# Kernel tuning notes

Measured on AMD Instinct MI355X. Metric: run time of the kernel, lower is better.

Reference implementation:

```python
import jax, jax.numpy as jnp
import numpy as np
import math

CH = 64  # channel

def setup_inputs() -> dict:
    key = jax.random.key(0)
    ks = jax.random.split(key, 7)
    B, K, M = 4, 32, 8192
    grouped_xyz = jax.random.normal(ks[0], (B, 3, K, M), dtype=jnp.float32)
    s = 1.0 / math.sqrt(3.0)
    Wq = jax.random.uniform(ks[1], (CH, 3), jnp.float32, -s, s)
    bq = jax.random.uniform(ks[2], (CH,), jnp.float32, -s, s)
    Wk = jax.random.uniform(ks[3], (CH, 3), jnp.float32, -s, s)
    bk = jax.random.uniform(ks[4], (CH,), jnp.float32, -s, s)
    Wv = jax.random.uniform(ks[5], (CH, 3), jnp.float32, -s, s)
    bv = jax.random.uniform(ks[6], (CH,), jnp.float32, -s, s)
    return {"grouped_xyz": grouped_xyz, "Wq": Wq, "bq": bq, "Wk": Wk, "bk": bk, "Wv": Wv, "bv": bv}

def reference(grouped_xyz, Wq, bq, Wk, bk, Wv, bv):
    # 1x1 conv = channel-wise linear: (B,3,K,M) -> (B,M,K,CH) after permute (0,3,2,1)
    def proj(W, b):
        return jnp.einsum('oc,bckm->bmko', W, grouped_xyz) + b
    q = proj(Wq, bq)  # B,M,K,C
    k = proj(Wk, bk)
    v = proj(Wv, bv)
    score = jnp.einsum('bmkc,bmjc->bmkj', q, k) / math.sqrt(CH)
    attn = jax.nn.softmax(score, axis=-1)
    pe = jax.nn.relu(jnp.einsum('bmkj,bmjc->bmkc', attn, v))  # B,M,K,C
    return pe
```

## Files before the change

### kernel.cpp

```cpp
#include <hip/hip_runtime.h>
#include <cstdint>

#define M_TOT 8192
#define K_PTS 32
#define NCH 64
#define MT 16

__global__ void setup_kernel(const float* __restrict__ Wq, const float* __restrict__ bq,
                             const float* __restrict__ Wk, const float* __restrict__ bk,
                             float* __restrict__ ws) {
  if (threadIdx.x == 0 && blockIdx.x == 0) {
    const float scale = 1.4426950408889634f / 8.0f;
    float A[9] = {0,0,0,0,0,0,0,0,0};
    float u[3] = {0,0,0};
    for (int o = 0; o < NCH; ++o) {
      float wq0 = Wq[o*3+0], wq1 = Wq[o*3+1], wq2 = Wq[o*3+2];
      float wk0 = Wk[o*3+0], wk1 = Wk[o*3+1], wk2 = Wk[o*3+2];
      float bqo = bq[o];
      A[0] += wq0*wk0; A[1] += wq0*wk1; A[2] += wq0*wk2;
      A[3] += wq1*wk0; A[4] += wq1*wk1; A[5] += wq1*wk2;
      A[6] += wq2*wk0; A[7] += wq2*wk1; A[8] += wq2*wk2;
      u[0] += bqo*wk0; u[1] += bqo*wk1; u[2] += bqo*wk2;
    }
    for (int i = 0; i < 9; ++i) ws[i] = A[i] * scale;
    for (int i = 0; i < 3; ++i) ws[9+i] = u[i] * scale;
  }
}

__global__ __launch_bounds__(512) void attn_main(const float* __restrict__ xyz,
                                                 const float* __restrict__ Wv,
                                                 const float* __restrict__ bv,
                                                 const float* __restrict__ ws,
                                                 float* __restrict__ out) {
  __shared__ __align__(16) float x_lds[MT*97 + 4];
  __shared__ __align__(16) float gh_lds[MT*128];
  __shared__ __align__(16) float y_lds[MT*128];

  const int t = threadIdx.x;
  const int b = blockIdx.x >> 9;
  const int m0 = (blockIdx.x & 511) * MT;

  const float* xb = xyz + ((size_t)b * 3 * K_PTS) * M_TOT + m0;

  #pragma unroll
  for (int p = 0; p < 3; ++p) {
    int i = t + p * 512;
    int mo = i & (MT - 1);
    int r  = i >> 4;
    float val = xb[(size_t)r * M_TOT + mo];
    int k = r & 31, c = r >> 5;
    x_lds[mo*97 + k*3 + c] = val;
  }

  float A00 = ws[0], A01 = ws[1], A02 = ws[2];
  float A10 = ws[3], A11 = ws[4], A12 = ws[5];
  float A20 = ws[6], A21 = ws[7], A22 = ws[8];
  float u0  = ws[9], u1  = ws[10], u2 = ws[11];

  __syncthreads();

  {
    int m = t >> 5, j = t & 31;
    float x0 = x_lds[m*97 + j*3 + 0];
    float x1 = x_lds[m*97 + j*3 + 1];
    float x2 = x_lds[m*97 + j*3 + 2];
    float g0 = fmaf(A02, x2, fmaf(A01, x1, A00 * x0));
    float g1 = fmaf(A12, x2, fmaf(A11, x1, A10 * x0));
    float g2 = fmaf(A22, x2, fmaf(A21, x1, A20 * x0));
    float h  = fmaf(u2,  x2, fmaf(u1,  x1, u0  * x0));
    *(float4*)&gh_lds[m*128 + j*4] = make_float4(g0, g1, g2, h);
  }
  __syncthreads();

  {
    int m = t >> 5, k = t & 31;
    float xk0 = x_lds[m*97 + k*3 + 0];
    float xk1 = x_lds[m*97 + k*3 + 1];
    float xk2 = x_lds[m*97 + k*3 + 2];
    float s[32];
    #pragma unroll
    for (int j = 0; j < 32; ++j) {
      float4 gh = *(const float4*)&gh_lds[m*128 + j*4];
      s[j] = fmaf(xk0, gh.x, fmaf(xk1, gh.y, fmaf(xk2, gh.z, gh.w)));
    }
    float mx = s[0];
    #pragma unroll
    for (int j = 1; j < 32; ++j) mx = fmaxf(mx, s[j]);
    float sum = 0.f, y0 = 0.f, y1 = 0.f, y2 = 0.f;
    #pragma unroll
    for (int j = 0; j < 32; ++j) {
      float p = exp2f(s[j] - mx);
      sum += p;
      y0 = fmaf(p, x_lds[m*97 + j*3 + 0], y0);
      y1 = fmaf(p, x_lds[m*97 + j*3 + 1], y1);
      y2 = fmaf(p, x_lds[m*97 + j*3 + 2], y2);
    }
    float inv = 1.0f / sum;
    *(float4*)&y_lds[m*128 + k*4] = make_float4(y0*inv, y1*inv, y2*inv, 0.f);
  }
  __syncthreads();

  {
    int k  = t >> 4;
    int c4 = (t & 15) * 4;
    float w00 = Wv[(c4+0)*3+0], w01 = Wv[(c4+0)*3+1], w02 = Wv[(c4+0)*3+2], b0 = bv[c4+0];
    float w10 = Wv[(c4+1)*3+0], w11 = Wv[(c4+1)*3+1], w12 = Wv[(c4+1)*3+2], b1 = bv[c4+1];
    float w20 = Wv[(c4+2)*3+0], w21 = Wv[(c4+2)*3+1], w22 = Wv[(c4+2)*3+2], b2 = bv[c4+2];
    float w30 = Wv[(c4+3)*3+0], w31 = Wv[(c4+3)*3+1], w32 = Wv[(c4+3)*3+2], b3 = bv[c4+3];
    float* op = out + (((size_t)b * M_TOT + m0) * K_PTS + k) * NCH + c4;
    #pragma unroll
    for (int m = 0; m < MT; ++m) {
      float4 y = *(const float4*)&y_lds[m*128 + k*4];
      float4 r;
      r.x = fmaxf(0.f, fmaf(w00, y.x, fmaf(w01, y.y, fmaf(w02, y.z, b0))));
      r.y = fmaxf(0.f, fmaf(w10, y.x, fmaf(w11, y.y, fmaf(w12, y.z, b1))));
      r.z = fmaxf(0.f, fmaf(w20, y.x, fmaf(w21, y.y, fmaf(w22, y.z, b2))));
      r.w = fmaxf(0.f, fmaf(w30, y.x, fmaf(w31, y.y, fmaf(w32, y.z, b3))));
      *(float4*)(op + (size_t)m * (K_PTS * NCH)) = r;
    }
  }
}

extern "C" void kernel_launch(void* const* d_in, const int* in_sizes, int n_in,
                              void* d_out, int out_size, void* d_ws, size_t ws_size,
                              hipStream_t stream) {
  const float* xyz = (const float*)d_in[0];
  const float* Wq  = (const float*)d_in[1];
  const float* bq  = (const float*)d_in[2];
  const float* Wk  = (const float*)d_in[3];
  const float* bk  = (const float*)d_in[4];
  const float* Wv  = (const float*)d_in[5];
  const float* bv  = (const float*)d_in[6];
  float* out = (float*)d_out;
  float* ws  = (float*)d_ws;

  setup_kernel<<<1, 64, 0, stream>>>(Wq, bq, Wk, bk, ws);
  attn_main<<<2048, 512, 0, stream>>>(xyz, Wv, bv, ws, out);
}
```

Measured before the change: 60.69 us.

## Fuse weight-precompute into main kernel and shrink tile to 8 points

Removes the single-thread setup kernel by having every block compute the folded Wq^T Wk matrix and bias vector via wavefront xor-shuffle reductions, eliminating one launch and its serialization. The tile is halved to 8 points with 256-thread blocks (4096 blocks), scores are recomputed in a second pass instead of held in a 32-entry register array, and output stores become nontemporal. This trades redundant per-block reduction work and recomputed dot products for lower register pressure, more blocks, and no inter-kernel dependency.

```diff
diff --git a/kernel.cpp b/kernel.cpp
--- a/kernel.cpp
+++ b/kernel.cpp
@@ -4,59 +4,67 @@
 #define M_TOT 8192
 #define K_PTS 32
 #define NCH 64
-#define MT 16
+#define MT 8
 
-__global__ void setup_kernel(const float* __restrict__ Wq, const float* __restrict__ bq,
-                             const float* __restrict__ Wk, const float* __restrict__ bk,
-                             float* __restrict__ ws) {
-  if (threadIdx.x == 0 && blockIdx.x == 0) {
-    const float scale = 1.4426950408889634f / 8.0f;
-    float A[9] = {0,0,0,0,0,0,0,0,0};
-    float u[3] = {0,0,0};
-    for (int o = 0; o < NCH; ++o) {
-      float wq0 = Wq[o*3+0], wq1 = Wq[o*3+1], wq2 = Wq[o*3+2];
-      float wk0 = Wk[o*3+0], wk1 = Wk[o*3+1], wk2 = Wk[o*3+2];
-      float bqo = bq[o];
-      A[0] += wq0*wk0; A[1] += wq0*wk1; A[2] += wq0*wk2;
-      A[3] += wq1*wk0; A[4] += wq1*wk1; A[5] += wq1*wk2;
-      A[6] += wq2*wk0; A[7] += wq2*wk1; A[8] += wq2*wk2;
-      u[0] += bqo*wk0; u[1] += bqo*wk1; u[2] += bqo*wk2;
-    }
-    for (int i = 0; i < 9; ++i) ws[i] = A[i] * scale;
-    for (int i = 0; i < 3; ++i) ws[9+i] = u[i] * scale;
-  }
-}
+typedef float f4 __attribute__((ext_vector_type(4)));
 
-__global__ __launch_bounds__(512) void attn_main(const float* __restrict__ xyz,
-                                                 const float* __restrict__ Wv,
-                                                 const float* __restrict__ bv,
-                                                 const float* __restrict__ ws,
-                                                 float* __restrict__ out) {
+__global__ __launch_bounds__(256) void attn_fused(const float* __restrict__ xyz,
+                                                  const float* __restrict__ Wq,
+                                                  const float* __restrict__ bq,
+                                                  const float* __restrict__ Wk,
+                                                  const float* __restrict__ Wv,
+                                                  const float* __restrict__ bv,
+                                                  float* __restrict__ out) {
   __shared__ __align__(16) float x_lds[MT*97 + 4];
   __shared__ __align__(16) float gh_lds[MT*128];
   __shared__ __align__(16) float y_lds[MT*128];
 
   const int t = threadIdx.x;
-  const int b = blockIdx.x >> 9;
-  const int m0 = (blockIdx.x & 511) * MT;
+  const int b = blockIdx.x >> 10;
+  const int m0 = (blockIdx.x & 1023) * MT;
 
   const float* xb = xyz + ((size_t)b * 3 * K_PTS) * M_TOT + m0;
 
+  float xv[3];
+  int rr[3], mm[3];
   #pragma unroll
   for (int p = 0; p < 3; ++p) {
-    int i = t + p * 512;
-    int mo = i & (MT - 1);
-    int r  = i >> 4;
-    float val = xb[(size_t)r * M_TOT + mo];
-    int k = r & 31, c = r >> 5;
-    x_lds[mo*97 + k*3 + c] = val;
+    int i = t + p * 256;
+    mm[p] = i & (MT - 1);
+    rr[p] = i >> 3;
+    xv[p] = xb[(size_t)rr[p] * M_TOT + mm[p]];
   }
 
-  float A00 = ws[0], A01 = ws[1], A02 = ws[2];
-  float A10 = ws[3], A11 = ws[4], A12 = ws[5];
-  float A20 = ws[6], A21 = ws[7], A22 = ws[8];
-  float u0  = ws[9], u1  = ws[10], u2 = ws[11];
+  const int c4 = (t & 15) * 4;
+  float w00 = Wv[(c4+0)*3+0], w01 = Wv[(c4+0)*3+1], w02 = Wv[(c4+0)*3+2], bv0 = bv[c4+0];
+  float w10 = Wv[(c4+1)*3+0], w11 = Wv[(c4+1)*3+1], w12 = Wv[(c4+1)*3+2], bv1 = bv[c4+1];
+  float w20 = Wv[(c4+2)*3+0], w21 = Wv[(c4+2)*3+1], w22 = Wv[(c4+2)*3+2], bv2 = bv[c4+2];
+  float w30 = Wv[(c4+3)*3+0], w31 = Wv[(c4+3)*3+1], w32 = Wv[(c4+3)*3+2], bv3 = bv[c4+3];
 
+  const int o = t & 63;
+  float wq0 = Wq[o*3+0], wq1 = Wq[o*3+1], wq2 = Wq[o*3+2];
+  float wk0 = Wk[o*3+0], wk1 = Wk[o*3+1], wk2 = Wk[o*3+2];
+  float bqo = bq[o];
+  float A00 = wq0*wk0, A01 = wq0*wk1, A02 = wq0*wk2;
+  float A10 = wq1*wk0, A11 = wq1*wk1, A12 = wq1*wk2;
+  float A20 = wq2*wk0, A21 = wq2*wk1, A22 = wq2*wk2;
+  float u0 = bqo*wk0, u1 = bqo*wk1, u2 = bqo*wk2;
+  #pragma unroll
+  for (int st = 1; st < 64; st <<= 1) {
+    A00 += __shfl_xor(A00, st); A01 += __shfl_xor(A01, st); A02 += __shfl_xor(A02, st);
+    A10 += __shfl_xor(A10, st); A11 += __shfl_xor(A11, st); A12 += __shfl_xor(A12, st);
+    A20 += __shfl_xor(A20, st); A21 += __shfl_xor(A21, st); A22 += __shfl_xor(A22, st);
+    u0  += __shfl_xor(u0,  st); u1  += __shfl_xor(u1,  st); u2  += __shfl_xor(u2,  st);
+  }
+  const float sc = 1.4426950408889634f / 8.0f;
+  A00 *= sc; A01 *= sc; A02 *= sc; A10 *= sc; A11 *= sc; A12 *= sc;
+  A20 *= sc; A21 *= sc; A22 *= sc; u0 *= sc; u1 *= sc; u2 *= sc;
+
+  #pragma unroll
+  for (int p = 0; p < 3; ++p) {
+    int k = rr[p] & 31, c = rr[p] >> 5;
+    x_lds[mm[p]*97 + k*3 + c] = xv[p];
+  }
   __syncthreads();
 
   {
@@ -68,7 +76,7 @@
     float g1 = fmaf(A12, x2, fmaf(A11, x1, A10 * x0));
     float g2 = fmaf(A22, x2, fmaf(A21, x1, A20 * x0));
     float h  = fmaf(u2,  x2, fmaf(u1,  x1, u0  * x0));
-    *(float4*)&gh_lds[m*128 + j*4] = make_float4(g0, g1, g2, h);
+    *(f4*)&gh_lds[m*128 + j*4] = (f4){g0, g1, g2, h};
   }
   __syncthreads();
 
@@ -77,46 +85,44 @@
     float xk0 = x_lds[m*97 + k*3 + 0];
     float xk1 = x_lds[m*97 + k*3 + 1];
     float xk2 = x_lds[m*97 + k*3 + 2];
-    float s[32];
+    float mx = -3.4e38f;
     #pragma unroll
     for (int j = 0; j < 32; ++j) {
-      float4 gh = *(const float4*)&gh_lds[m*128 + j*4];
-      s[j] = fmaf(xk0, gh.x, fmaf(xk1, gh.y, fmaf(xk2, gh.z, gh.w)));
+      f4 gh = *(const f4*)&gh_lds[m*128 + j*4];
+      float s = fmaf(xk0, gh.x, fmaf(xk1, gh.y, fmaf(xk2, gh.z, gh.w)));
+      mx = fmaxf(mx, s);
     }
-    float mx = s[0];
-    #pragma unroll
-    for (int j = 1; j < 32; ++j) mx = fmaxf(mx, s[j]);
     float sum = 0.f, y0 = 0.f, y1 = 0.f, y2 = 0.f;
     #pragma unroll
     for (int j = 0; j < 32; ++j) {
-      float p = exp2f(s[j] - mx);
+      f4 gh = *(const f4*)&gh_lds[m*128 + j*4];
+      float s = fmaf(xk0, gh.x, fmaf(xk1, gh.y, fmaf(xk2, gh.z, gh.w)));
+      float p = exp2f(s - mx);
       sum += p;
       y0 = fmaf(p, x_lds[m*97 + j*3 + 0], y0);
       y1 = fmaf(p, x_lds[m*97 + j*3 + 1], y1);
       y2 = fmaf(p, x_lds[m*97 + j*3 + 2], y2);
     }
     float inv = 1.0f / sum;
-    *(float4*)&y_lds[m*128 + k*4] = make_float4(y0*inv, y1*inv, y2*inv, 0.f);
+    *(f4*)&y_lds[m*128 + k*4] = (f4){y0*inv, y1*inv, y2*inv, 0.f};
   }
   __syncthreads();
 
   {
-    int k  = t >> 4;
-    int c4 = (t & 15) * 4;
-    float w00 = Wv[(c4+0)*3+0], w01 = Wv[(c4+0)*3+1], w02 = Wv[(c4+0)*3+2], b0 = bv[c4+0];
-    float w10 = Wv[(c4+1)*3+0], w11 = Wv[(c4+1)*3+1], w12 = Wv[(c4+1)*3+2], b1 = bv[c4+1];
-    float w20 = Wv[(c4+2)*3+0], w21 = Wv[(c4+2)*3+1], w22 = Wv[(c4+2)*3+2], b2 = bv[c4+2];
-    float w30 = Wv[(c4+3)*3+0], w31 = Wv[(c4+3)*3+1], w32 = Wv[(c4+3)*3+2], b3 = bv[c4+3];
-    float* op = out + (((size_t)b * M_TOT + m0) * K_PTS + k) * NCH + c4;
+    float* op = out + (((size_t)b * M_TOT + m0) * K_PTS) * NCH + c4;
     #pragma unroll
     for (int m = 0; m < MT; ++m) {
-      float4 y = *(const float4*)&y_lds[m*128 + k*4];
-      float4 r;
-      r.x = fmaxf(0.f, fmaf(w00, y.x, fmaf(w01, y.y, fmaf(w02, y.z, b0))));
-      r.y = fmaxf(0.f, fmaf(w10, y.x, fmaf(w11, y.y, fmaf(w12, y.z, b1))));
-      r.z = fmaxf(0.f, fmaf(w20, y.x, fmaf(w21, y.y, fmaf(w22, y.z, b2))));
-      r.w = fmaxf(0.f, fmaf(w30, y.x, fmaf(w31, y.y, fmaf(w32, y.z, b3))));
-      *(float4*)(op + (size_t)m * (K_PTS * NCH)) = r;
+      #pragma unroll
+      for (int h = 0; h < 2; ++h) {
+        int k = (t >> 4) + h * 16;
+        f4 y = *(const f4*)&y_lds[m*128 + k*4];
+        f4 r;
+        r.x = fmaxf(0.f, fmaf(w00, y.x, fmaf(w01, y.y, fmaf(w02, y.z, bv0))));
+        r.y = fmaxf(0.f, fmaf(w10, y.x, fmaf(w11, y.y, fmaf(w12, y.z, bv1))));
+        r.z = fmaxf(0.f, fmaf(w20, y.x, fmaf(w21, y.y, fmaf(w22, y.z, bv2))));
+        r.w = fmaxf(0.f, fmaf(w30, y.x, fmaf(w31, y.y, fmaf(w32, y.z, bv3))));
+        __builtin_nontemporal_store(r, (f4*)(op + ((size_t)m * K_PTS + k) * NCH));
+      }
     }
   }
 }
@@ -128,12 +134,9 @@
   const float* Wq  = (const float*)d_in[1];
   const float* bq  = (const float*)d_in[2];
   const float* Wk  = (const float*)d_in[3];
-  const float* bk  = (const float*)d_in[4];
   const float* Wv  = (const float*)d_in[5];
   const float* bv  = (const float*)d_in[6];
   float* out = (float*)d_out;
-  float* ws  = (float*)d_ws;
 
-  setup_kernel<<<1, 64, 0, stream>>>(Wq, bq, Wk, bk, ws);
-  attn_main<<<2048, 512, 0, stream>>>(xyz, Wv, bv, ws, out);
+  attn_fused<<<4096, 256, 0, stream>>>(xyz, Wq, bq, Wk, Wv, bv, out);
 }
```

Result: slower. 62.96 us (+3.7%).
